# Performance work log

Measured on AMD Instinct MI355X. Metric: run time of the kernel, lower is better.

## Reference

```python
import jax, jax.numpy as jnp
import numpy as np

# GConvLSTM (torch_geometric_temporal) single step, H=None,C=None -> zeros.
# Each gate g uses two ChebConvs: conv_x_g(X) + conv_h_g(H) + (w_c_g*C for i,f; only i,f,o have w_c) + b_g
# With H=C=0: gate preact = conv_x_g(X) + conv_h_g(0) + b_g. ChebConv(0)=0 only if bias=False;
# torch_geometric_temporal ChebConvs use bias=True by default, so conv_h_g(0) = bias_h_g (a vector).
# We fold conv_h bias into b. Cheb recursion with sym norm, lambda_max=2 default in ChebConv? Actually
# ChebConv requires lambda_max or normalization='sym' default uses lambda_max=2.0 assumption:
# Tx_0 = x; Tx_1 = L_hat @ x where L_hat = -D^-1/2 A D^-1/2 (since L_scaled = L - I = -A_norm for lambda_max=2);
# Tx_k = 2*L_hat@Tx_{k-1} - Tx_{k-2}. out = sum_k Tx_k @ W_k + bias.

MULT = 2
IN_CH = 10
WIDTHS = [8 * MULT, 16 * MULT, 32 * MULT, 76 * MULT]
KS = [2, 3, 4, 5]
NUM_CLASSES = 2
N_NODES = 100000
N_EDGES = 3200000


def _norm_adj(edge_index, n):
    src, dst = edge_index[0], edge_index[1]
    deg = jax.ops.segment_sum(jnp.ones_like(src, dtype=jnp.float32), dst, num_segments=n)
    dinv = jnp.where(deg > 0, jax.lax.rsqrt(jnp.maximum(deg, 1.0)), 0.0)
    w = dinv[src] * dinv[dst]  # [E]
    return src, dst, w


def _lhat_mul(x, src, dst, w, n):
    # L_hat @ x = -A_norm @ x  (lambda_max=2, sym norm, no self loops added in scaled L beyond -I cancel)
    msg = x[src] * w[:, None]  # [E,F]
    agg = jax.ops.segment_sum(msg, dst, num_segments=n)
    return -agg


def cheb_conv(x, Ws, b, src, dst, w, n):
    # Ws: [K, F_in, F_out]
    K = Ws.shape[0]
    Tx0 = x
    out = Tx0 @ Ws[0]
    if K > 1:
        Tx1 = _lhat_mul(Tx0, src, dst, w, n)
        out = out + Tx1 @ Ws[1]
        for k in range(2, K):
            Tx2 = 2.0 * _lhat_mul(Tx1, src, dst, w, n) - Tx0
            out = out + Tx2 @ Ws[k]
            Tx0, Tx1 = Tx1, Tx2
    return out + b


def gconv_lstm_step(x, params, src, dst, w, n):
    # params: dict with per-gate Wx,Wh (cheb weights), bx,bh, b, and w_ci,w_cf,w_co
    def conv_pair(g):
        cx = cheb_conv(x, params[f'Wx_{g}'], params[f'bx_{g}'], src, dst, w, n)
        # H = 0 => conv_h contributes only its bias
        return cx + params[f'bh_{g}'] + params[f'b_{g}']
    # C = 0 => peephole terms w_c*C vanish
    i = jax.nn.sigmoid(conv_pair('i'))
    f = jax.nn.sigmoid(conv_pair('f'))
    c = i * jnp.tanh(conv_pair('c'))
    o = jax.nn.sigmoid(conv_pair('o'))
    h = o * jnp.tanh(c)
    return h


def _make_layer_params(key, f_in, f_out, K):
    p = {}
    ks = jax.random.split(key, 16)
    scale = 1.0 / np.sqrt(f_in * K)
    for gi, g in enumerate(['i', 'f', 'c', 'o']):
        p[f'Wx_{g}'] = jax.random.normal(ks[4 * gi], (K, f_in, f_out), jnp.float32) * scale
        p[f'bx_{g}'] = jnp.zeros((f_out,), jnp.float32)
        p[f'bh_{g}'] = jnp.zeros((f_out,), jnp.float32)
        p[f'b_{g}'] = jnp.zeros((f_out,), jnp.float32)
    return p


def setup_inputs() -> dict:
    key = jax.random.key(0)
    kx, ke, kp, kl = jax.random.split(key, 4)
    x = jax.random.normal(kx, (N_NODES, IN_CH), jnp.float32)
    edge_index = jax.random.randint(ke, (2, N_EDGES), 0, N_NODES, dtype=jnp.int64)
    layer_keys = jax.random.split(kp, 4)
    params = []
    f_in = IN_CH
    for li, (f_out, K) in enumerate(zip(WIDTHS, KS)):
        params.append(_make_layer_params(layer_keys[li], f_in, f_out, K))
        f_in = f_out
    flat = {}
    for li, p in enumerate(params):
        for k, v in p.items():
            flat[f'l{li}_{k}'] = v
    kw, kb = jax.random.split(kl)
    flat['lin_W'] = jax.random.normal(kw, (WIDTHS[-1], NUM_CLASSES), jnp.float32) * (1.0 / np.sqrt(WIDTHS[-1]))
    flat['lin_b'] = jnp.zeros((NUM_CLASSES,), jnp.float32)
    return {'x': x, 'edge_index': edge_index, **flat}


_GATE_KEYS = [f'{pre}_{g}' for g in ['i', 'f', 'c', 'o'] for pre in ['Wx', 'bx', 'bh', 'b']]


def _forward(x, edge_index, params_by_layer, lin_W, lin_b):
    n = x.shape[0]
    src, dst, w = _norm_adj(edge_index, n)
    h = x
    for p in params_by_layer:
        h = gconv_lstm_step(h, p, src, dst, w, n)
        h = jax.nn.relu(h)  # dropout: eval mode -> identity
    logits = h @ lin_W + lin_b
    return jax.nn.softmax(logits, axis=-1)


def reference(x, edge_index,
              l0_Wx_i, l0_bx_i, l0_bh_i, l0_b_i, l0_Wx_f, l0_bx_f, l0_bh_f, l0_b_f, l0_Wx_c, l0_bx_c, l0_bh_c, l0_b_c, l0_Wx_o, l0_bx_o, l0_bh_o, l0_b_o,
              l1_Wx_i, l1_bx_i, l1_bh_i, l1_b_i, l1_Wx_f, l1_bx_f, l1_bh_f, l1_b_f, l1_Wx_c, l1_bx_c, l1_bh_c, l1_b_c, l1_Wx_o, l1_bx_o, l1_bh_o, l1_b_o,
              l2_Wx_i, l2_bx_i, l2_bh_i, l2_b_i, l2_Wx_f, l2_bx_f, l2_bh_f, l2_b_f, l2_Wx_c, l2_bx_c, l2_bh_c, l2_b_c, l2_Wx_o, l2_bx_o, l2_bh_o, l2_b_o,
              l3_Wx_i, l3_bx_i, l3_bh_i, l3_b_i, l3_Wx_f, l3_bx_f, l3_bh_f, l3_b_f, l3_Wx_c, l3_bx_c, l3_bh_c, l3_b_c, l3_Wx_o, l3_bx_o, l3_bh_o, l3_b_o,
              lin_W, lin_b):
    loc = locals()
    params_by_layer = []
    for li in range(4):
        params_by_layer.append({k: loc[f'l{li}_{k}'] for k in _GATE_KEYS})
    return _forward(x, edge_index, params_by_layer, lin_W, lin_b)
```

## Files before the change

### kernel.cpp

```cpp
#include <hip/hip_runtime.h>


#define IN_CH 10
#define PCH 128
#define NB2MAX 512
typedef unsigned short u16;
typedef unsigned long long u64;
typedef short bf16x8 __attribute__((ext_vector_type(8)));
typedef float f32x4 __attribute__((ext_vector_type(4)));

struct __align__(8) Edge { int s; float w; };

__device__ __forceinline__ float bf2f(u16 u) { return __uint_as_float(((unsigned)u) << 16); }
__device__ __forceinline__ float lo16f(unsigned v) { return __uint_as_float(v << 16); }
__device__ __forceinline__ float hi16f(unsigned v) { return __uint_as_float(v & 0xffff0000u); }
__device__ __forceinline__ u16 f2bf(float f) {
    unsigned x = __float_as_uint(f);
    return (u16)((x + 0x7fff + ((x >> 16) & 1)) >> 16);
}
__device__ __forceinline__ float ldv(const float* p) { return *p; }
__device__ __forceinline__ float ldv(const u16* p) { return bf2f(*p); }
__device__ __forceinline__ void stv(float* p, float v) { *p = v; }
__device__ __forceinline__ void stv(u16* p, float v) { *p = f2bf(v); }

__device__ __forceinline__ void gload16(const u16* g, u16* l) {
    __builtin_amdgcn_global_load_lds(
        (const __attribute__((address_space(1))) unsigned*)(const void*)g,
        (__attribute__((address_space(3))) unsigned*)(void*)l, 16, 0, 0);
}


__global__ __launch_bounds__(256) void k_bcount(const int* __restrict__ dst,
                                                int* __restrict__ C, int e, int nb2) {
    __shared__ int sh[NB2MAX];
    const int p = blockIdx.x;
    for (int i = threadIdx.x; i < nb2; i += 256) sh[i] = 0;
    __syncthreads();
    const int chunk = (e + PCH - 1) / PCH;
    const int e0 = p * chunk, e1 = min(e0 + chunk, e);
    for (int i = e0 + threadIdx.x; i < e1; i += 256)
        atomicAdd(&sh[dst[i] >> 8], 1);
    __syncthreads();
    for (int b = threadIdx.x; b < nb2; b += 256) C[b * PCH + p] = sh[b];
}

__global__ __launch_bounds__(512) void k_boff(int* __restrict__ C, int* __restrict__ seg,
                                              int nb2) {
    __shared__ int sh[512];
    const int t = threadIdx.x;
    int tot = 0;
    if (t < nb2) {
        int* Cb = C + (size_t)t * PCH;
        int run = 0;
#pragma unroll 4
        for (int p = 0; p < PCH; p++) { int v = Cb[p]; Cb[p] = run; run += v; }
        tot = run;
    }
    sh[t] = tot;
    __syncthreads();
    for (int off = 1; off < 512; off <<= 1) {
        int x = (t >= off) ? sh[t - off] : 0;
        __syncthreads();
        sh[t] += x;
        __syncthreads();
    }
    const int base = sh[t] - tot;
    if (t < nb2) {
        seg[t] = base;
        int* Cb = C + (size_t)t * PCH;
#pragma unroll 4
        for (int p = 0; p < PCH; p++) Cb[p] += base;
        if (t == nb2 - 1) seg[nb2] = base + tot;
    }
}

__global__ __launch_bounds__(256) void k_stage(const int* __restrict__ src,
                                               const int* __restrict__ dst,
                                               const int* __restrict__ C,
                                               int* __restrict__ Sd, int* __restrict__ Ss,
                                               int e, int nb2) {
    __shared__ int cur[NB2MAX];
    const int p = blockIdx.x;
    for (int i = threadIdx.x; i < nb2; i += 256) cur[i] = C[(size_t)i * PCH + p];
    __syncthreads();
    const int chunk = (e + PCH - 1) / PCH;
    const int e0 = p * chunk, e1 = min(e0 + chunk, e);
    for (int i = e0 + threadIdx.x; i < e1; i += 256) {
        int d = dst[i], s = src[i];
        int pos = atomicAdd(&cur[d >> 8], 1);
        Sd[pos] = d;
        Ss[pos] = s;
    }
}

__global__ __launch_bounds__(256) void k_bknt(const int* __restrict__ Sd,
                                              const int* __restrict__ seg,
                                              int* __restrict__ cnt, int n) {
    __shared__ int sh[256];
    const int b = blockIdx.x;
    sh[threadIdx.x] = 0;
    __syncthreads();
    const int lo = seg[b], hi = seg[b + 1];
    for (int i = lo + threadIdx.x; i < hi; i += 256)
        atomicAdd(&sh[Sd[i] & 255], 1);
    __syncthreads();
    int node = b * 256 + threadIdx.x;
    if (node < n) cnt[node] = sh[threadIdx.x];
}

__global__ __launch_bounds__(256) void k_bscat(const int* __restrict__ Sd,
                                               const int* __restrict__ Ss,
                                               const int* __restrict__ seg,
                                               const int* __restrict__ row_ptr,
                                               const float* __restrict__ dinv,
                                               Edge* __restrict__ ed, int n) {
    __shared__ int cur[256];
    const int b = blockIdx.x;
    int node = b * 256 + threadIdx.x;
    cur[threadIdx.x] = node < n ? row_ptr[node] : 0;
    __syncthreads();
    const int lo = seg[b], hi = seg[b + 1];
    for (int i = lo + threadIdx.x; i < hi; i += 256) {
        int d = Sd[i], s = Ss[i];
        int pos = atomicAdd(&cur[d & 255], 1);
        float w = dinv[s] * dinv[d];
        u64 v = (u64)(unsigned)s | ((u64)__float_as_uint(w) << 32);
        *(u64*)&ed[pos] = v;
    }
}

__global__ void k_dinv(const int* __restrict__ cnt, float* __restrict__ dinv, int n) {
    int i = blockIdx.x * 256 + threadIdx.x;
    if (i < n) dinv[i] = cnt[i] > 0 ? rsqrtf((float)cnt[i]) : 0.f;
}


__global__ void k_bsum(const int* __restrict__ cnt, int* __restrict__ bsum, int n) {
    __shared__ int red[256];
    int t = threadIdx.x;
    int idx = blockIdx.x * 1024 + t * 4;
    int s = 0;
#pragma unroll
    for (int j = 0; j < 4; j++) s += (idx + j < n) ? cnt[idx + j] : 0;
    red[t] = s;
    __syncthreads();
    for (int off = 128; off > 0; off >>= 1) {
        if (t < off) red[t] += red[t + off];
        __syncthreads();
    }
    if (t == 0) bsum[blockIdx.x] = red[0];
}

__global__ __launch_bounds__(1024) void k_bscan(const int* __restrict__ bsum,
                                                int* __restrict__ boff,
                                                int* __restrict__ total_out, int B) {
    __shared__ int sh[1024];
    int t = threadIdx.x;
    int v = t < B ? bsum[t] : 0;
    sh[t] = v;
    __syncthreads();
    for (int off = 1; off < 1024; off <<= 1) {
        int x = (t >= off) ? sh[t - off] : 0;
        __syncthreads();
        sh[t] += x;
        __syncthreads();
    }
    if (t < B) boff[t] = sh[t] - v;
    if (t == B - 1) *total_out = sh[t];
}

__global__ void k_write(const int* __restrict__ cnt, const int* __restrict__ boff,
                        int* __restrict__ row_ptr, int* __restrict__ cursor, int n) {
    __shared__ int tsum[256];
    int t = threadIdx.x;
    int idx = blockIdx.x * 1024 + t * 4;
    int c[4];
    int s = 0;
#pragma unroll
    for (int j = 0; j < 4; j++) {
        c[j] = (idx + j < n) ? cnt[idx + j] : 0;
        s += c[j];
    }
    tsum[t] = s;
    __syncthreads();
    for (int off = 1; off < 256; off <<= 1) {
        int x = (t >= off) ? tsum[t - off] : 0;
        __syncthreads();
        tsum[t] += x;
        __syncthreads();
    }
    int run = boff[blockIdx.x] + tsum[t] - s;
#pragma unroll
    for (int j = 0; j < 4; j++) {
        if (idx + j < n) {
            row_ptr[idx + j] = run;
            cursor[idx + j] = run;
            run += c[j];
        }
    }
}


template <int F>
__global__ void k_spmv(const u16* __restrict__ X, const u16* __restrict__ Tprev,
                       u16* __restrict__ Tout, const int* __restrict__ row_ptr,
                       const Edge* __restrict__ ed, int n, float scale) {
    int lane = threadIdx.x;
    int node = blockIdx.x * blockDim.y + threadIdx.y;
    if (node >= n) return;
    int lo = row_ptr[node], hi = row_ptr[node + 1];
    const u16* Xc = X + 2 * lane;
    float a0[4] = {0.f, 0.f, 0.f, 0.f};
    float a1[4] = {0.f, 0.f, 0.f, 0.f};
    int e = lo;
    for (; e + 8 <= hi; e += 8) {
        Edge q[8];
#pragma unroll
        for (int j = 0; j < 8; j++) q[j] = ed[e + j];
        unsigned v[8];
#pragma unroll
        for (int j = 0; j < 8; j++)
            v[j] = *(const unsigned*)(Xc + (size_t)q[j].s * F);
#pragma unroll
        for (int j = 0; j < 8; j++) {
            a0[j & 3] = fmaf(q[j].w, lo16f(v[j]), a0[j & 3]);
            a1[j & 3] = fmaf(q[j].w, hi16f(v[j]), a1[j & 3]);
        }
    }
    for (; e + 4 <= hi; e += 4) {
        Edge q[4];
#pragma unroll
        for (int j = 0; j < 4; j++) q[j] = ed[e + j];
        unsigned v[4];
#pragma unroll
        for (int j = 0; j < 4; j++)
            v[j] = *(const unsigned*)(Xc + (size_t)q[j].s * F);
#pragma unroll
        for (int j = 0; j < 4; j++) {
            a0[j] = fmaf(q[j].w, lo16f(v[j]), a0[j]);
            a1[j] = fmaf(q[j].w, hi16f(v[j]), a1[j]);
        }
    }
    for (; e < hi; e++) {
        Edge q = ed[e];
        unsigned v = *(const unsigned*)(Xc + (size_t)q.s * F);
        a0[0] = fmaf(q.w, lo16f(v), a0[0]);
        a1[0] = fmaf(q.w, hi16f(v), a1[0]);
    }
    float v0 = -scale * ((a0[0] + a0[1]) + (a0[2] + a0[3]));
    float v1 = -scale * ((a1[0] + a1[1]) + (a1[2] + a1[3]));
    if (Tprev) {
        unsigned pv = *(const unsigned*)(Tprev + (size_t)node * F + 2 * lane);
        v0 -= lo16f(pv);
        v1 -= hi16f(pv);
    }
    *(unsigned*)(Tout + (size_t)node * F + 2 * lane) =
        (unsigned)f2bf(v0) | ((unsigned)f2bf(v1) << 16);
}

struct TP { const void* p[5]; };

template <typename ST, int FIN, int K>
__global__ __launch_bounds__(256) void k_chebgate(TP tp, const float* __restrict__ Wp,
                                                  const float* __restrict__ b4,
                                                  ST* __restrict__ H, int n, int F,
                                                  int F4pad) {
    __shared__ float As[FIN][68];
    __shared__ float Ws[FIN][128];
    const int tid = threadIdx.x;
    const int fx = tid & 31, ry = tid >> 5;
    const int row0 = blockIdx.y * 64;
    const int f0 = blockIdx.x * 32;
    const int f = f0 + fx;

    float acc[8][3];
    const float4 bv = *(const float4*)&b4[(size_t)f * 4];
#pragma unroll
    for (int r = 0; r < 8; r++) { acc[r][0] = bv.x; acc[r][1] = bv.y; acc[r][2] = bv.z; }

#pragma unroll
    for (int t = 0; t < K; t++) {
        const ST* T = (const ST*)tp.p[t];
        for (int idx = tid; idx < 64 * FIN; idx += 256) {
            int r = idx / FIN, a = idx - r * FIN;
            int rr = row0 + r;
            if (rr >= n) rr = n - 1;
            As[a][r] = ldv(&T[(size_t)rr * FIN + a]);
        }
        const float* Wt = Wp + (size_t)t * FIN * F4pad + (size_t)f0 * 4;
        for (int idx = tid; idx < FIN * 128; idx += 256) {
            int aa = idx >> 7, c = idx & 127;
            Ws[aa][c] = Wt[(size_t)aa * F4pad + c];
        }
        __syncthreads();
#pragma unroll 2
        for (int a = 0; a < FIN; a++) {
            const float4 w = *(const float4*)&Ws[a][fx * 4];
            const float4 x0 = *(const float4*)&As[a][ry * 8];
            const float4 x1 = *(const float4*)&As[a][ry * 8 + 4];
            const float xr[8] = {x0.x, x0.y, x0.z, x0.w, x1.x, x1.y, x1.z, x1.w};
#pragma unroll
            for (int r = 0; r < 8; r++) {
                acc[r][0] = fmaf(xr[r], w.x, acc[r][0]);
                acc[r][1] = fmaf(xr[r], w.y, acc[r][1]);
                acc[r][2] = fmaf(xr[r], w.z, acc[r][2]);
            }
        }
        __syncthreads();
    }

    if (f < F) {
#pragma unroll
        for (int r = 0; r < 8; r++) {
            int row = row0 + ry * 8 + r;
            if (row < n) {
                float gi = 1.f / (1.f + __expf(-acc[r][0]));
                float go = 1.f / (1.f + __expf(-acc[r][2]));
                float c = gi * tanhf(acc[r][1]);
                float h = go * tanhf(c);
                stv(&H[(size_t)row * F + f], fmaxf(h, 0.f));
            }
        }
    }
}


template <int FIN, int K, int NT, int FPAD>
__global__ __launch_bounds__(256) void k_chebgate_mfma2(TP tp, const u16* __restrict__ Bp,
                                                        const float* __restrict__ b3,
                                                        u16* __restrict__ H, int n, int F,
                                                        int Hstride) {
    constexpr int NIT = K * FIN / 32;
    constexpr int CPR = FIN / 8;
    constexpr int CSH = (CPR == 8) ? 3 : 2;
    constexpr int PANEL = 128 * FIN;
    constexpr int IPT = (128 * CPR) / 256;
    __shared__ __align__(16) u16 Alds[K * PANEL];

    const int tid = threadIdx.x;
    const int xb = blockIdx.x;
    const int wv = tid >> 6, lane = tid & 63;
    const int ln = lane & 15, lk = lane >> 4;
    const size_t panel_g = (size_t)xb * 128 * FIN;

#pragma unroll
    for (int t = 0; t < K; t++) {
        const u16* g = (const u16*)tp.p[t] + panel_g;
#pragma unroll
        for (int i = 0; i < IPT; i++) {
            int j0 = wv * (IPT * 64) + i * 64;
            int j = j0 + lane;
            int row = j >> CSH, c = j & (CPR - 1);
            int sc = (j & ~(CPR - 1)) | (c ^ (row & (CPR - 1)));
            gload16(g + (size_t)sc * 8, Alds + (size_t)t * PANEL + (size_t)j0 * 8);
        }
    }
    __syncthreads();

    const int r0 = xb * 128 + wv * 32;
    const u16* Bl = Bp + (size_t)lane * 8;

#pragma unroll 1
    for (int yb = 0; yb < NT; yb++) {
        f32x4 acc[2][2][3];
#pragma unroll
        for (int rt = 0; rt < 2; rt++)
#pragma unroll
            for (int s = 0; s < 2; s++)
#pragma unroll
                for (int g = 0; g < 3; g++) acc[rt][s][g] = (f32x4){0.f, 0.f, 0.f, 0.f};

#pragma unroll
        for (int it = 0; it < NIT; it++) {
            const int k0 = it * 32;
            const int t = k0 / FIN;
            const int a0 = k0 % FIN;
            bf16x8 af[2];
#pragma unroll
            for (int rt = 0; rt < 2; rt++) {
                int lrow = wv * 32 + rt * 16 + ln;
                int kc = (a0 >> 3) + lk;
                int kcs = kc ^ (lrow & (CPR - 1));
                af[rt] = *(const bf16x8*)(Alds + (size_t)t * PANEL + (size_t)lrow * FIN + kcs * 8);
            }
#pragma unroll
            for (int s = 0; s < 2; s++)
#pragma unroll
                for (int g = 0; g < 3; g++) {
                    int fi = (yb * NIT + it) * 6 + s * 3 + g;
                    bf16x8 bf = *(const bf16x8*)(Bl + (size_t)fi * 512);
#pragma unroll
                    for (int rt = 0; rt < 2; rt++)
                        acc[rt][s][g] = __builtin_amdgcn_mfma_f32_16x16x32_bf16(
                            af[rt], bf, acc[rt][s][g], 0, 0, 0);
                }
        }

        const int f0 = yb * 32;
#pragma unroll
        for (int s = 0; s < 2; s++) {
            int fcol = f0 + s * 16 + ln;
            if (fcol >= F) continue;
            float bi = b3[0 * FPAD + fcol];
            float bc = b3[1 * FPAD + fcol];
            float bo = b3[2 * FPAD + fcol];
#pragma unroll
            for (int rt = 0; rt < 2; rt++) {
#pragma unroll
                for (int reg = 0; reg < 4; reg++) {
                    int row = r0 + rt * 16 + lk * 4 + reg;
                    if (row < n) {
                        float gi = 1.f / (1.f + __expf(-(acc[rt][s][0][reg] + bi)));
                        float go = 1.f / (1.f + __expf(-(acc[rt][s][2][reg] + bo)));
                        float c = gi * tanhf(acc[rt][s][1][reg] + bc);
                        float h = go * tanhf(c);
                        H[(size_t)row * Hstride + fcol] = f2bf(fmaxf(h, 0.f));
                    }
                }
            }
        }
    }
}


template <int FIN, int K, int NT, int FPAD>
__global__ __launch_bounds__(256) void k_chebgate_mfma_fused2(
    TP tp, const u16* __restrict__ Bp, const float* __restrict__ b3,
    const float* __restrict__ W2, float* __restrict__ part, int n, int F) {
    constexpr int NIT = K * FIN / 32;
    constexpr int CPR = FIN / 8;
    constexpr int CSH = (CPR == 8) ? 3 : 2;
    constexpr int PANEL = 128 * FIN;
    constexpr int IPT = (128 * CPR) / 256;
    __shared__ __align__(16) u16 Alds[K * PANEL];

    const int tid = threadIdx.x;
    const int xb = blockIdx.x;
    const int wv = tid >> 6, lane = tid & 63;
    const int ln = lane & 15, lk = lane >> 4;
    const size_t panel_g = (size_t)xb * 128 * FIN;

#pragma unroll
    for (int t = 0; t < K; t++) {
        const u16* g = (const u16*)tp.p[t] + panel_g;
#pragma unroll
        for (int i = 0; i < IPT; i++) {
            int j0 = wv * (IPT * 64) + i * 64;
            int j = j0 + lane;
            int row = j >> CSH, c = j & (CPR - 1);
            int sc = (j & ~(CPR - 1)) | (c ^ (row & (CPR - 1)));
            gload16(g + (size_t)sc * 8, Alds + (size_t)t * PANEL + (size_t)j0 * 8);
        }
    }
    __syncthreads();

    const int r0 = xb * 128 + wv * 32;
    const u16* Bl = Bp + (size_t)lane * 8;

#pragma unroll 1
    for (int yb = 0; yb < NT; yb++) {
        f32x4 acc[2][2][3];
#pragma unroll
        for (int rt = 0; rt < 2; rt++)
#pragma unroll
            for (int s = 0; s < 2; s++)
#pragma unroll
                for (int g = 0; g < 3; g++) acc[rt][s][g] = (f32x4){0.f, 0.f, 0.f, 0.f};

#pragma unroll
        for (int it = 0; it < NIT; it++) {
            const int k0 = it * 32;
            const int t = k0 / FIN;
            const int a0 = k0 % FIN;
            bf16x8 af[2];
#pragma unroll
            for (int rt = 0; rt < 2; rt++) {
                int lrow = wv * 32 + rt * 16 + ln;
                int kc = (a0 >> 3) + lk;
                int kcs = kc ^ (lrow & (CPR - 1));
                af[rt] = *(const bf16x8*)(Alds + (size_t)t * PANEL + (size_t)lrow * FIN + kcs * 8);
            }
#pragma unroll
            for (int s = 0; s < 2; s++)
#pragma unroll
                for (int g = 0; g < 3; g++) {
                    int fi = (yb * NIT + it) * 6 + s * 3 + g;
                    bf16x8 bf = *(const bf16x8*)(Bl + (size_t)fi * 512);
#pragma unroll
                    for (int rt = 0; rt < 2; rt++)
                        acc[rt][s][g] = __builtin_amdgcn_mfma_f32_16x16x32_bf16(
                            af[rt], bf, acc[rt][s][g], 0, 0, 0);
                }
        }

        const int f0 = yb * 32;
        float p0[2][4], p1[2][4];
#pragma unroll
        for (int rt = 0; rt < 2; rt++)
#pragma unroll
            for (int reg = 0; reg < 4; reg++) { p0[rt][reg] = 0.f; p1[rt][reg] = 0.f; }

#pragma unroll
        for (int s = 0; s < 2; s++) {
            int fcol = f0 + s * 16 + ln;
            float w20 = fcol < F ? W2[fcol * 2 + 0] : 0.f;
            float w21 = fcol < F ? W2[fcol * 2 + 1] : 0.f;
            float bi = b3[0 * FPAD + fcol];
            float bc = b3[1 * FPAD + fcol];
            float bo = b3[2 * FPAD + fcol];
#pragma unroll
            for (int rt = 0; rt < 2; rt++) {
#pragma unroll
                for (int reg = 0; reg < 4; reg++) {
                    float gi = 1.f / (1.f + __expf(-(acc[rt][s][0][reg] + bi)));
                    float go = 1.f / (1.f + __expf(-(acc[rt][s][2][reg] + bo)));
                    float c = gi * tanhf(acc[rt][s][1][reg] + bc);
                    float h = fmaxf(go * tanhf(c), 0.f);
                    p0[rt][reg] = fmaf(h, w20, p0[rt][reg]);
                    p1[rt][reg] = fmaf(h, w21, p1[rt][reg]);
                }
            }
        }

#pragma unroll
        for (int rt = 0; rt < 2; rt++) {
#pragma unroll
            for (int reg = 0; reg < 4; reg++) {
                float v0 = p0[rt][reg], v1 = p1[rt][reg];
#pragma unroll
                for (int m = 1; m <= 8; m <<= 1) {
                    v0 += __shfl_xor(v0, m);
                    v1 += __shfl_xor(v1, m);
                }
                p0[rt][reg] = v0;
                p1[rt][reg] = v1;
            }
        }

        if (ln == 0) {
#pragma unroll
            for (int rt = 0; rt < 2; rt++) {
#pragma unroll
                for (int reg = 0; reg < 4; reg++) {
                    int row = r0 + rt * 16 + lk * 4 + reg;
                    if (row < n) {
                        float* pp = part + ((size_t)yb * n + row) * 2;
                        pp[0] = p0[rt][reg];
                        pp[1] = p1[rt][reg];
                    }
                }
            }
        }
    }
}

__global__ void k_smax(const float* __restrict__ part, const float* __restrict__ b,
                       float* __restrict__ out, int n, int ntiles) {
    int i = blockIdx.x * 256 + threadIdx.x;
    if (i >= n) return;
    float l0 = b[0], l1 = b[1];
    for (int t = 0; t < ntiles; t++) {
        const float* pp = part + ((size_t)t * n + i) * 2;
        l0 += pp[0];
        l1 += pp[1];
    }
    float m = fmaxf(l0, l1);
    float e0 = __expf(l0 - m), e1 = __expf(l1 - m);
    float s = 1.f / (e0 + e1);
    out[(size_t)i * 2 + 0] = e0 * s;
    out[(size_t)i * 2 + 1] = e1 * s;
}


__global__ void k_pack_w(const float* __restrict__ Wi, const float* __restrict__ Wc,
                         const float* __restrict__ Wo, float* __restrict__ Wp,
                         int KFIN, int F, int F4pad) {
    int idx = blockIdx.x * 256 + threadIdx.x;
    int tot = KFIN * F4pad;
    if (idx >= tot) return;
    int c = idx % F4pad;
    int ka = idx / F4pad;
    int f = c >> 2, g = c & 3;
    float v = 0.f;
    if (g < 3 && f < F) {
        const float* Wg = (g == 0) ? Wi : ((g == 1) ? Wc : Wo);
        v = Wg[(size_t)ka * F + f];
    }
    Wp[idx] = v;
}

__global__ void k_pack_b(const float* __restrict__ bxi, const float* __restrict__ bhi,
                         const float* __restrict__ bi, const float* __restrict__ bxc,
                         const float* __restrict__ bhc, const float* __restrict__ bc,
                         const float* __restrict__ bxo, const float* __restrict__ bho,
                         const float* __restrict__ bo, float* __restrict__ b4,
                         int F, int F4pad) {
    int idx = blockIdx.x * 256 + threadIdx.x;
    if (idx >= F4pad) return;
    int f = idx >> 2, g = idx & 3;
    float v = 0.f;
    if (g < 3 && f < F) {
        if (g == 0) v = bxi[f] + bhi[f] + bi[f];
        else if (g == 1) v = bxc[f] + bhc[f] + bc[f];
        else v = bxo[f] + bho[f] + bo[f];
    }
    b4[idx] = v;
}

__global__ void k_pack_wf(const float* __restrict__ Wi, const float* __restrict__ Wc,
                          const float* __restrict__ Wo, u16* __restrict__ Bp,
                          int NIT, int Fin, int F, int NT) {
    int idx = blockIdx.x * 256 + threadIdx.x;
    int tot = NT * NIT * 6 * 512;
    if (idx >= tot) return;
    int frag = idx >> 9;
    int r = idx & 511;
    int lane = r >> 3, j = r & 7;
    int lk = lane >> 4, ln = lane & 15;
    int yb = frag / (NIT * 6);
    int q = frag % (NIT * 6);
    int it = q / 6, sg = q % 6;
    int s = sg / 3, g = sg % 3;
    int fcol = yb * 32 + s * 16 + ln;
    int k = it * 32 + lk * 8 + j;
    int t = k / Fin, a = k % Fin;
    float v = 0.f;
    if (fcol < F) {
        const float* Wg = (g == 0) ? Wi : ((g == 1) ? Wc : Wo);
        v = Wg[((size_t)t * Fin + a) * F + fcol];
    }
    Bp[idx] = f2bf(v);
}

__global__ void k_pack_b3(const float* __restrict__ bxi, const float* __restrict__ bhi,
                          const float* __restrict__ bi, const float* __restrict__ bxc,
                          const float* __restrict__ bhc, const float* __restrict__ bc,
                          const float* __restrict__ bxo, const float* __restrict__ bho,
                          const float* __restrict__ bo, float* __restrict__ b3,
                          int F, int FPAD) {
    int idx = blockIdx.x * 256 + threadIdx.x;
    if (idx >= 3 * FPAD) return;
    int g = idx / FPAD, f = idx % FPAD;
    float v = 0.f;
    if (f < F) {
        if (g == 0) v = bxi[f] + bhi[f] + bi[f];
        else if (g == 1) v = bxc[f] + bhc[f] + bc[f];
        else v = bxo[f] + bho[f] + bo[f];
    }
    b3[idx] = v;
}

__global__ void k_cvt(const float* __restrict__ x, u16* __restrict__ y, int n) {
    int i = blockIdx.x * 256 + threadIdx.x;
    if (i < n) y[i] = f2bf(x[i]);
}


static inline size_t al(size_t x) { return (x + 255) & ~(size_t)255; }

extern "C" void kernel_launch(void* const* d_in, const int* in_sizes, int n_in,
                              void* d_out, int out_size, void* d_ws, size_t ws_size,
                              hipStream_t stream) {
    const float* X0 = (const float*)d_in[0];
    const int* ei = (const int*)d_in[1];
    const int N = in_sizes[0] / IN_CH;
    const int E = in_sizes[1] / 2;
    const int* src = ei;
    const int* dst = ei + E;

    char* p = (char*)d_ws;
    size_t off = 0;
    auto carve = [&](size_t bytes) -> char* { char* r = p + off; off += al(bytes); return r; };
    int* row_ptr  = (int*)carve((size_t)(N + 1) * 4);
    int* cnt      = (int*)carve((size_t)N * 4);
    int* cursor   = (int*)carve((size_t)N * 4);
    float* dinv   = (float*)carve((size_t)N * 4);
    int* bsum     = (int*)carve((size_t)1024 * 4);
    int* boff     = (int*)carve((size_t)1024 * 4);
    int* Cb       = (int*)carve((size_t)NB2MAX * PCH * 4);
    int* seg      = (int*)carve((size_t)(NB2MAX + 1) * 4);
    Edge* edges   = (Edge*)carve((size_t)E * 8);
    const size_t S64 = al((size_t)N * 64 * 2);
    char* bufA    = carve(5 * S64);
    char* bufB    = carve((size_t)N * 304);
    float* Wp     = (float*)carve((size_t)48 * 128 * 4);
    float* b4     = (float*)carve((size_t)128 * 4);
    u16* Wt       = (u16*)carve((size_t)480 * 320 * 2);
    float* b3     = (float*)carve((size_t)480 * 4);
    (void)ws_size;

    u16* X0c  = (u16*)bufA;
    u16* T0_1 = (u16*)(bufA + al((size_t)N * 20));
    u16* H0   = (u16*)(bufA + S64);
    u16* T1_1 = (u16*)(bufA + S64 + al((size_t)N * 32));
    u16* T1_2 = (u16*)(bufA + S64 + 2 * al((size_t)N * 32));
    u16* L2T[4];
    for (int t = 0; t < 4; t++) L2T[t] = (u16*)(bufB + t * al((size_t)N * 64));
    u16* L3T[5];
    for (int t = 0; t < 5; t++) L3T[t] = (u16*)(bufA + t * S64);
    float* part = (float*)bufB;
    int* Sd = (int*)bufA;
    int* Ss = (int*)(bufA + al((size_t)E * 4));

    int gN = (N + 255) / 256;
    int B = (N + 1023) / 1024;
    int nb2 = (N + 255) / 256;
    k_bcount<<<PCH, 256, 0, stream>>>(dst, Cb, E, nb2);
    k_boff<<<1, 512, 0, stream>>>(Cb, seg, nb2);
    k_stage<<<PCH, 256, 0, stream>>>(src, dst, Cb, Sd, Ss, E, nb2);
    k_bknt<<<nb2, 256, 0, stream>>>(Sd, seg, cnt, N);
    k_dinv<<<gN, 256, 0, stream>>>(cnt, dinv, N);
    k_bsum<<<B, 256, 0, stream>>>(cnt, bsum, N);
    k_bscan<<<1, 1024, 0, stream>>>(bsum, boff, row_ptr + N, B);
    k_write<<<B, 256, 0, stream>>>(cnt, boff, row_ptr, cursor, N);
    k_bscat<<<nb2, 256, 0, stream>>>(Sd, Ss, seg, row_ptr, dinv, edges, N);

    k_cvt<<<(N * IN_CH + 255) / 256, 256, 0, stream>>>(X0, X0c, N * IN_CH);

    dim3 gv(1, (N + 63) / 64);
    int rb = (N + 127) / 128;

    dim3 bs5(5, 48);   int g5 = (N + 47) / 48;
    dim3 bs8(8, 32);   int g8 = (N + 31) / 32;
    dim3 bs16(16, 16); int g16 = (N + 15) / 16;
    dim3 bs32(32, 8);  int g32 = (N + 7) / 8;

    {
        k_pack_w<<<(20 * 128 + 255) / 256, 256, 0, stream>>>(
            (const float*)d_in[2], (const float*)d_in[10], (const float*)d_in[14], Wp, 20, 16, 128);
        k_pack_b<<<1, 256, 0, stream>>>(
            (const float*)d_in[3], (const float*)d_in[4], (const float*)d_in[5],
            (const float*)d_in[11], (const float*)d_in[12], (const float*)d_in[13],
            (const float*)d_in[15], (const float*)d_in[16], (const float*)d_in[17], b4, 16, 128);
        k_spmv<10><<<g5, bs5, 0, stream>>>(X0c, nullptr, T0_1, row_ptr, edges, N, 1.f);
        TP tp; tp.p[0] = X0c; tp.p[1] = T0_1;
        k_chebgate<u16, 10, 2><<<gv, 256, 0, stream>>>(tp, Wp, b4, H0, N, 16, 128);
    }
    {
        k_pack_w<<<(48 * 128 + 255) / 256, 256, 0, stream>>>(
            (const float*)d_in[18], (const float*)d_in[26], (const float*)d_in[30], Wp, 48, 32, 128);
        k_pack_b<<<1, 256, 0, stream>>>(
            (const float*)d_in[19], (const float*)d_in[20], (const float*)d_in[21],
            (const float*)d_in[27], (const float*)d_in[28], (const float*)d_in[29],
            (const float*)d_in[31], (const float*)d_in[32], (const float*)d_in[33], b4, 32, 128);
        k_spmv<16><<<g8, bs8, 0, stream>>>(H0, nullptr, T1_1, row_ptr, edges, N, 1.f);
        k_spmv<16><<<g8, bs8, 0, stream>>>(T1_1, H0, T1_2, row_ptr, edges, N, 2.f);
        TP tp; tp.p[0] = H0; tp.p[1] = T1_1; tp.p[2] = T1_2;
        k_chebgate<u16, 16, 3><<<gv, 256, 0, stream>>>(tp, Wp, b4, L2T[0], N, 32, 128);
    }
    {
        k_pack_wf<<<(2 * 4 * 6 * 512 + 255) / 256, 256, 0, stream>>>(
            (const float*)d_in[34], (const float*)d_in[42], (const float*)d_in[46], Wt, 4, 32, 64, 2);
        k_pack_b3<<<1, 256, 0, stream>>>(
            (const float*)d_in[35], (const float*)d_in[36], (const float*)d_in[37],
            (const float*)d_in[43], (const float*)d_in[44], (const float*)d_in[45],
            (const float*)d_in[47], (const float*)d_in[48], (const float*)d_in[49], b3, 64, 64);
        k_spmv<32><<<g16, bs16, 0, stream>>>(L2T[0], nullptr, L2T[1], row_ptr, edges, N, 1.f);
        k_spmv<32><<<g16, bs16, 0, stream>>>(L2T[1], L2T[0], L2T[2], row_ptr, edges, N, 2.f);
        k_spmv<32><<<g16, bs16, 0, stream>>>(L2T[2], L2T[1], L2T[3], row_ptr, edges, N, 2.f);
        TP tp; for (int t = 0; t < 4; t++) tp.p[t] = L2T[t];
        k_chebgate_mfma2<32, 4, 2, 64><<<rb, 256, 0, stream>>>(tp, Wt, b3, L3T[0], N, 64, 64);
    }
    {
        k_pack_wf<<<(5 * 10 * 6 * 512 + 255) / 256, 256, 0, stream>>>(
            (const float*)d_in[50], (const float*)d_in[58], (const float*)d_in[62], Wt, 10, 64, 152, 5);
        k_pack_b3<<<2, 256, 0, stream>>>(
            (const float*)d_in[51], (const float*)d_in[52], (const float*)d_in[53],
            (const float*)d_in[59], (const float*)d_in[60], (const float*)d_in[61],
            (const float*)d_in[63], (const float*)d_in[64], (const float*)d_in[65], b3, 152, 160);
        k_spmv<64><<<g32, bs32, 0, stream>>>(L3T[0], nullptr, L3T[1], row_ptr, edges, N, 1.f);
        k_spmv<64><<<g32, bs32, 0, stream>>>(L3T[1], L3T[0], L3T[2], row_ptr, edges, N, 2.f);
        k_spmv<64><<<g32, bs32, 0, stream>>>(L3T[2], L3T[1], L3T[3], row_ptr, edges, N, 2.f);
        k_spmv<64><<<g32, bs32, 0, stream>>>(L3T[3], L3T[2], L3T[4], row_ptr, edges, N, 2.f);
        TP tp; for (int t = 0; t < 5; t++) tp.p[t] = L3T[t];
        k_chebgate_mfma_fused2<64, 5, 5, 160><<<rb, 256, 0, stream>>>(
            tp, Wt, b3, (const float*)d_in[66], part, N, 152);
    }

    k_smax<<<gN, 256, 0, stream>>>(part, (const float*)d_in[67], (float*)d_out, N, 5);
}
```

Baseline: 1.033 ms.

## Use 512-thread blocks in fused gate kernel and fast exp-based tanh

The final-layer fused Chebyshev gate kernel now runs 512 threads (8 waves) per 128-row tile, so each wave handles 16 rows instead of 32. This halves the accumulator registers per wave and should raise occupancy and latency hiding, at the cost of each wave re-reading the B fragments for fewer MFMAs. Separately, tanhf is replaced everywhere with an __expf-based formula, which is cheaper but may lose some accuracy or overflow to inf for large inputs (the formula still returns 1 in that case).

```diff
diff --git a/kernel.cpp b/kernel.cpp
--- a/kernel.cpp
+++ b/kernel.cpp
@@ -22,6 +22,11 @@
 __device__ __forceinline__ float ldv(const u16* p) { return bf2f(*p); }
 __device__ __forceinline__ void stv(float* p, float v) { *p = v; }
 __device__ __forceinline__ void stv(u16* p, float v) { *p = f2bf(v); }
+
+__device__ __forceinline__ float ftanh(float x) {
+    float t = __expf(2.f * x);
+    return 1.f - 2.f / (t + 1.f);
+}
 
 __device__ __forceinline__ void gload16(const u16* g, u16* l) {
     __builtin_amdgcn_global_load_lds(
@@ -316,8 +321,8 @@
             if (row < n) {
                 float gi = 1.f / (1.f + __expf(-acc[r][0]));
                 float go = 1.f / (1.f + __expf(-acc[r][2]));
-                float c = gi * tanhf(acc[r][1]);
-                float h = go * tanhf(c);
+                float c = gi * ftanh(acc[r][1]);
+                float h = go * ftanh(c);
                 stv(&H[(size_t)row * F + f], fmaxf(h, 0.f));
             }
         }
@@ -412,8 +417,8 @@
                     if (row < n) {
                         float gi = 1.f / (1.f + __expf(-(acc[rt][s][0][reg] + bi)));
                         float go = 1.f / (1.f + __expf(-(acc[rt][s][2][reg] + bo)));
-                        float c = gi * tanhf(acc[rt][s][1][reg] + bc);
-                        float h = go * tanhf(c);
+                        float c = gi * ftanh(acc[rt][s][1][reg] + bc);
+                        float h = go * ftanh(c);
                         H[(size_t)row * Hstride + fcol] = f2bf(fmaxf(h, 0.f));
                     }
                 }
@@ -424,14 +429,14 @@
 
 
 template <int FIN, int K, int NT, int FPAD>
-__global__ __launch_bounds__(256) void k_chebgate_mfma_fused2(
+__global__ __launch_bounds__(512, 4) void k_chebgate_mfma_fused2(
     TP tp, const u16* __restrict__ Bp, const float* __restrict__ b3,
     const float* __restrict__ W2, float* __restrict__ part, int n, int F) {
     constexpr int NIT = K * FIN / 32;
     constexpr int CPR = FIN / 8;
     constexpr int CSH = (CPR == 8) ? 3 : 2;
     constexpr int PANEL = 128 * FIN;
-    constexpr int IPT = (128 * CPR) / 256;
+    constexpr int IPT = (128 * CPR) / 512;
     __shared__ __align__(16) u16 Alds[K * PANEL];
 
     const int tid = threadIdx.x;
@@ -454,51 +459,41 @@
     }
     __syncthreads();
 
-    const int r0 = xb * 128 + wv * 32;
+    const int r0 = xb * 128 + wv * 16;
+    const int lrow = wv * 16 + ln;
+    const int rmask = lrow & (CPR - 1);
     const u16* Bl = Bp + (size_t)lane * 8;
 
 #pragma unroll 1
     for (int yb = 0; yb < NT; yb++) {
-        f32x4 acc[2][2][3];
-#pragma unroll
-        for (int rt = 0; rt < 2; rt++)
-#pragma unroll
-            for (int s = 0; s < 2; s++)
-#pragma unroll
-                for (int g = 0; g < 3; g++) acc[rt][s][g] = (f32x4){0.f, 0.f, 0.f, 0.f};
+        f32x4 acc[2][3];
+#pragma unroll
+        for (int s = 0; s < 2; s++)
+#pragma unroll
+            for (int g = 0; g < 3; g++) acc[s][g] = (f32x4){0.f, 0.f, 0.f, 0.f};
 
 #pragma unroll
         for (int it = 0; it < NIT; it++) {
             const int k0 = it * 32;
             const int t = k0 / FIN;
             const int a0 = k0 % FIN;
-            bf16x8 af[2];
-#pragma unroll
-            for (int rt = 0; rt < 2; rt++) {
-                int lrow = wv * 32 + rt * 16 + ln;
-                int kc = (a0 >> 3) + lk;
-                int kcs = kc ^ (lrow & (CPR - 1));
-                af[rt] = *(const bf16x8*)(Alds + (size_t)t * PANEL + (size_t)lrow * FIN + kcs * 8);
-            }
+            int kcs = ((a0 >> 3) + lk) ^ rmask;
+            bf16x8 af = *(const bf16x8*)(Alds + (size_t)t * PANEL + (size_t)lrow * FIN + kcs * 8);
 #pragma unroll
             for (int s = 0; s < 2; s++)
 #pragma unroll
                 for (int g = 0; g < 3; g++) {
                     int fi = (yb * NIT + it) * 6 + s * 3 + g;
                     bf16x8 bf = *(const bf16x8*)(Bl + (size_t)fi * 512);
-#pragma unroll
-                    for (int rt = 0; rt < 2; rt++)
-                        acc[rt][s][g] = __builtin_amdgcn_mfma_f32_16x16x32_bf16(
-                            af[rt], bf, acc[rt][s][g], 0, 0, 0);
+                    acc[s][g] = __builtin_amdgcn_mfma_f32_16x16x32_bf16(
+                        af, bf, acc[s][g], 0, 0, 0);
                 }
         }
 
         const int f0 = yb * 32;
-        float p0[2][4], p1[2][4];
-#pragma unroll
-        for (int rt = 0; rt < 2; rt++)
-#pragma unroll
-            for (int reg = 0; reg < 4; reg++) { p0[rt][reg] = 0.f; p1[rt][reg] = 0.f; }
+        float p0[4], p1[4];
+#pragma unroll
+        for (int reg = 0; reg < 4; reg++) { p0[reg] = 0.f; p1[reg] = 0.f; }
 
 #pragma unroll
         for (int s = 0; s < 2; s++) {
@@ -509,45 +504,36 @@
             float bc = b3[1 * FPAD + fcol];
             float bo = b3[2 * FPAD + fcol];
 #pragma unroll
-            for (int rt = 0; rt < 2; rt++) {
-#pragma unroll
-                for (int reg = 0; reg < 4; reg++) {
-                    float gi = 1.f / (1.f + __expf(-(acc[rt][s][0][reg] + bi)));
-                    float go = 1.f / (1.f + __expf(-(acc[rt][s][2][reg] + bo)));
-                    float c = gi * tanhf(acc[rt][s][1][reg] + bc);
-                    float h = fmaxf(go * tanhf(c), 0.f);
-                    p0[rt][reg] = fmaf(h, w20, p0[rt][reg]);
-                    p1[rt][reg] = fmaf(h, w21, p1[rt][reg]);
-                }
+            for (int reg = 0; reg < 4; reg++) {
+                float gi = 1.f / (1.f + __expf(-(acc[s][0][reg] + bi)));
+                float go = 1.f / (1.f + __expf(-(acc[s][2][reg] + bo)));
+                float c = gi * ftanh(acc[s][1][reg] + bc);
+                float h = fmaxf(go * ftanh(c), 0.f);
+                p0[reg] = fmaf(h, w20, p0[reg]);
+                p1[reg] = fmaf(h, w21, p1[reg]);
             }
         }
 
 #pragma unroll
-        for (int rt = 0; rt < 2; rt++) {
+        for (int reg = 0; reg < 4; reg++) {
+            float v0 = p0[reg], v1 = p1[reg];
+#pragma unroll
+            for (int m = 1; m <= 8; m <<= 1) {
+                v0 += __shfl_xor(v0, m);
+                v1 += __shfl_xor(v1, m);
+            }
+            p0[reg] = v0;
+            p1[reg] = v1;
+        }
+
+        if (ln == 0) {
 #pragma unroll
             for (int reg = 0; reg < 4; reg++) {
-                float v0 = p0[rt][reg], v1 = p1[rt][reg];
-#pragma unroll
-                for (int m = 1; m <= 8; m <<= 1) {
-                    v0 += __shfl_xor(v0, m);
-                    v1 += __shfl_xor(v1, m);
-                }
-                p0[rt][reg] = v0;
-                p1[rt][reg] = v1;
-            }
-        }
-
-        if (ln == 0) {
-#pragma unroll
-            for (int rt = 0; rt < 2; rt++) {
-#pragma unroll
-                for (int reg = 0; reg < 4; reg++) {
-                    int row = r0 + rt * 16 + lk * 4 + reg;
-                    if (row < n) {
-                        float* pp = part + ((size_t)yb * n + row) * 2;
-                        pp[0] = p0[rt][reg];
-                        pp[1] = p1[rt][reg];
-                    }
+                int row = r0 + lk * 4 + reg;
+                if (row < n) {
+                    float* pp = part + ((size_t)yb * n + row) * 2;
+                    pp[0] = p0[reg];
+                    pp[1] = p1[reg];
                 }
             }
         }
@@ -773,7 +759,7 @@
         k_spmv<64><<<g32, bs32, 0, stream>>>(L3T[2], L3T[1], L3T[3], row_ptr, edges, N, 2.f);
         k_spmv<64><<<g32, bs32, 0, stream>>>(L3T[3], L3T[2], L3T[4], row_ptr, edges, N, 2.f);
         TP tp; for (int t = 0; t < 5; t++) tp.p[t] = L3T[t];
-        k_chebgate_mfma_fused2<64, 5, 5, 160><<<rb, 256, 0, stream>>>(
+        k_chebgate_mfma_fused2<64, 5, 5, 160><<<rb, 512, 0, stream>>>(
             tp, Wt, b3, (const float*)d_in[66], part, N, 152);
     }
 
```

Result: no change. 1.028 ms, median of 2 (-0.5%).
